# Kernel optimization log

Measured on AMD Instinct MI355X. Metric: run time of the kernel, lower is better.

## Reference

```python
import jax, jax.numpy as jnp
import numpy as np
import math

D, H, NQP, NKP = 512, 8, 4, 4
DH = D // H
OUT_DIM = D + H * NKP * 3  # 608


def setup_inputs() -> dict:
    key = jax.random.key(0)
    ks = jax.random.split(key, 12)
    B, L = 2, 1024
    s = jax.random.normal(ks[0], (B, L, D), dtype=jnp.float32)
    R = jax.random.normal(ks[1], (B, L, 3, 3), dtype=jnp.float32)
    tr = jax.random.normal(ks[2], (B, L, 3), dtype=jnp.float32)
    sc = 0.02
    Wq = jax.random.normal(ks[3], (D, D), dtype=jnp.float32) * sc
    Wk = jax.random.normal(ks[4], (D, D), dtype=jnp.float32) * sc
    Wv = jax.random.normal(ks[5], (D, D), dtype=jnp.float32) * sc
    Wqp = jax.random.normal(ks[6], (D, H * NQP * 3), dtype=jnp.float32) * sc
    Wkp = jax.random.normal(ks[7], (D, H * NKP * 3), dtype=jnp.float32) * sc
    Wvp = jax.random.normal(ks[8], (D, H * NKP * 3), dtype=jnp.float32) * sc
    Wo = jax.random.normal(ks[9], (OUT_DIM, D), dtype=jnp.float32) * sc
    bo = jnp.zeros((D,), dtype=jnp.float32)
    gamma = jnp.ones((D,), dtype=jnp.float32)
    beta = jnp.zeros((D,), dtype=jnp.float32)
    w_C = jnp.full((H,), math.log(20.0), dtype=jnp.float32)
    return dict(s=s, R=R, tr=tr, Wq=Wq, Wk=Wk, Wv=Wv, Wqp=Wqp, Wkp=Wkp,
                Wvp=Wvp, Wo=Wo, bo=bo, gamma=gamma, beta=beta, w_C=w_C)


def _layernorm(x, gamma, beta, eps=1e-5):
    mu = jnp.mean(x, axis=-1, keepdims=True)
    var = jnp.var(x, axis=-1, keepdims=True)
    return (x - mu) * jax.lax.rsqrt(var + eps) * gamma + beta


def reference(s, R, tr, Wq, Wk, Wv, Wqp, Wkp, Wvp, Wo, bo, gamma, beta, w_C):
    B, L, _ = s.shape
    # scalar q/k/v: (B, L, H, dh)
    Q = (s @ Wq).reshape(B, L, H, DH)
    K = (s @ Wk).reshape(B, L, H, DH)
    V = (s @ Wv).reshape(B, L, H, DH)
    a_s = jnp.einsum('bihd,bjhd->bhij', Q, K) / math.sqrt(DH)
    # local points: (B, L, H, P, 3)
    Qp = (s @ Wqp).reshape(B, L, H, NQP, 3)
    Kp = (s @ Wkp).reshape(B, L, H, NKP, 3)
    Vp = (s @ Wvp).reshape(B, L, H, NKP, 3)
    tr_e = tr[:, :, None, None, :]
    to_global = lambda p: jnp.einsum('blxy,blhpy->blhpx', R, p) + tr_e
    Qp_g, Kp_g, Vp_g = to_global(Qp), to_global(Kp), to_global(Vp)
    # (B, H, L, P, 3)
    qh = jnp.transpose(Qp_g, (0, 2, 1, 3, 4))
    kh = jnp.transpose(Kp_g, (0, 2, 1, 3, 4))
    diff = qh[:, :, :, None] - kh[:, :, None]          # (B,H,L,L,P,3)
    sq_dist = jnp.sum(diff * diff, axis=(-2, -1))      # (B,H,L,L)
    wc = jax.nn.softplus(w_C)[None, :, None, None]
    attn = jax.nn.softmax(a_s - 0.5 * wc * sq_dist, axis=-1)
    out_s = jnp.einsum('bhij,bjhd->bihd', attn, V).reshape(B, L, D)
    Vp_agg = jnp.einsum('bhij,bjhpc->bihpc', attn, Vp_g)  # (B,L,H,P,3)
    # global -> local: R^T (p - tr)
    Vp_local = jnp.einsum('blyx,blhpy->blhpx', R, Vp_agg - tr_e)
    out_p = Vp_local.reshape(B, L, H * NKP * 3)
    out = jnp.concatenate([out_s, out_p], axis=-1) @ Wo + bo
    return _layernorm(s + out, gamma, beta)
```

## Files before the change

### kernel.cpp

```cpp
#include <hip/hip_runtime.h>
#include <hip/hip_fp16.h>
#include <math.h>

typedef _Float16 f16;
typedef _Float16 f16x8 __attribute__((ext_vector_type(8)));
typedef _Float16 f16x4v __attribute__((ext_vector_type(4)));
typedef float f32x4 __attribute__((ext_vector_type(4)));

#define BATCH   2
#define LSEQ    1024
#define BLTOT   2048
#define DMODEL  512
#define NHEAD   8
#define PDIM    1824
#define AW      96
#define VW      80
#define ODIM    608
#define NSPLIT  2
#define OCPSTR  1310720

__global__ __launch_bounds__(256)
void prep_kernel(const float* __restrict__ s,
                 const float* __restrict__ Wq, const float* __restrict__ Wk,
                 const float* __restrict__ Wv, const float* __restrict__ Wqp,
                 const float* __restrict__ Wkp, const float* __restrict__ Wvp,
                 f16* __restrict__ sH, f16* __restrict__ WallT)
{
    const int blk = blockIdx.x;
    const int t = threadIdx.x;
    __shared__ float tile[32][33];

    if (blk < 1024) {
        const int i = blk * 256 + t;
        float4 v = ((const float4*)s)[i];
        f16x4v o = { (f16)v.x, (f16)v.y, (f16)v.z, (f16)v.w };
        ((f16x4v*)sH)[i] = o;
        return;
    }
    {
        const int idx = blk - 1024;
        const int n0 = (idx % 57) * 32, k0 = (idx / 57) * 32;
        const float* src; int ld, nc0;
        if      (n0 < 512)  { src = Wq;  ld = 512; nc0 = n0; }
        else if (n0 < 1024) { src = Wk;  ld = 512; nc0 = n0 - 512; }
        else if (n0 < 1536) { src = Wv;  ld = 512; nc0 = n0 - 1024; }
        else if (n0 < 1632) { src = Wqp; ld = 96;  nc0 = n0 - 1536; }
        else if (n0 < 1728) { src = Wkp; ld = 96;  nc0 = n0 - 1632; }
        else                { src = Wvp; ld = 96;  nc0 = n0 - 1728; }
#pragma unroll
        for (int i = 0; i < 4; ++i) {
            const int idx2 = t + i * 256;
            const int kl = idx2 >> 5, nl = idx2 & 31;
            tile[kl][nl] = src[(long long)(k0 + kl) * ld + nc0 + nl];
        }
        __syncthreads();
#pragma unroll
        for (int i = 0; i < 4; ++i) {
            const int idx2 = t + i * 256;
            const int nl = idx2 >> 5, kl = idx2 & 31;
            WallT[(long long)(n0 + nl) * 512 + k0 + kl] = (f16)tile[kl][nl];
        }
    }
}

__global__ __launch_bounds__(256)
void proj_kernel(const f16* __restrict__ A, const f16* __restrict__ Bt,
                 const float* __restrict__ Wo, f16* __restrict__ WoT,
                 f16* __restrict__ P)
{
    __shared__ f16 As[2][64][40];
    __shared__ f16 Bs[2][96][40];
    const int t = threadIdx.x;

    if (blockIdx.y >= 32) {
        float (*tile)[33] = (float(*)[33])&As[0][0][0];
        const int base = (blockIdx.x + (blockIdx.y - 32) * 19) * 8;
#pragma unroll 1
        for (int it = 0; it < 8; ++it) {
            const int idx = base + it;
            const int n0 = (idx & 15) * 32, k0 = (idx >> 4) * 32;
#pragma unroll
            for (int i = 0; i < 4; ++i) {
                const int idx2 = t + i * 256;
                const int kl = idx2 >> 5, nl = idx2 & 31;
                tile[kl][nl] = Wo[(long long)(k0 + kl) * 512 + n0 + nl];
            }
            __syncthreads();
#pragma unroll
            for (int i = 0; i < 4; ++i) {
                const int idx2 = t + i * 256;
                const int nl = idx2 >> 5, kl = idx2 & 31;
                WoT[(long long)(n0 + nl) * 608 + k0 + kl] = (f16)tile[kl][nl];
            }
            __syncthreads();
        }
        return;
    }

    const int w = t >> 6, lane = t & 63, l15 = lane & 15, lhi = lane >> 4;
    const int row0 = blockIdx.y * 64, col0 = blockIdx.x * 96;
    const int ar = t >> 2, ac = t & 3;
    const int K = 512;

    f32x4 acc[6];
#pragma unroll
    for (int n = 0; n < 6; ++n) acc[n] = (f32x4){0.f, 0.f, 0.f, 0.f};

    f16x8 aR, bR[2];
    aR = *(const f16x8*)&A[(long long)(row0 + ar) * K + ac * 8];
#pragma unroll
    for (int i = 0; i < 2; ++i) {
        const int cid = t + i * 256;
        if (cid < 384) {
            const int br = cid >> 2, bc = cid & 3;
            bR[i] = *(const f16x8*)&Bt[(long long)(col0 + br) * K + bc * 8];
        }
    }
    *(f16x8*)&As[0][ar][ac * 8] = aR;
#pragma unroll
    for (int i = 0; i < 2; ++i) {
        const int cid = t + i * 256;
        if (cid < 384) *(f16x8*)&Bs[0][cid >> 2][(cid & 3) * 8] = bR[i];
    }
    __syncthreads();

    for (int st = 0; st < 16; ++st) {
        const int cur = st & 1;
        if (st + 1 < 16) {
            const int k0 = (st + 1) << 5;
            aR = *(const f16x8*)&A[(long long)(row0 + ar) * K + k0 + ac * 8];
#pragma unroll
            for (int i = 0; i < 2; ++i) {
                const int cid = t + i * 256;
                if (cid < 384) {
                    const int br = cid >> 2, bc = cid & 3;
                    bR[i] = *(const f16x8*)&Bt[(long long)(col0 + br) * K + k0 + bc * 8];
                }
            }
        }
        f16x8 af = *(const f16x8*)&As[cur][w * 16 + l15][lhi * 8];
        f16x8 bf[6];
#pragma unroll
        for (int n = 0; n < 6; ++n)
            bf[n] = *(const f16x8*)&Bs[cur][n * 16 + l15][lhi * 8];
#pragma unroll
        for (int n = 0; n < 6; ++n)
            acc[n] = __builtin_amdgcn_mfma_f32_16x16x32_f16(af, bf[n], acc[n], 0, 0, 0);
        if (st + 1 < 16) {
            *(f16x8*)&As[cur ^ 1][ar][ac * 8] = aR;
#pragma unroll
            for (int i = 0; i < 2; ++i) {
                const int cid = t + i * 256;
                if (cid < 384) *(f16x8*)&Bs[cur ^ 1][cid >> 2][(cid & 3) * 8] = bR[i];
            }
        }
        __syncthreads();
    }

    const int row = row0 + w * 16 + lhi * 4;
#pragma unroll
    for (int n = 0; n < 6; ++n) {
        const int col = col0 + n * 16 + l15;
#pragma unroll
        for (int r = 0; r < 4; ++r)
            P[(long long)(row + r) * PDIM + col] = (f16)acc[n][r];
    }
}

template<int BN, bool OUT16>
__global__ __launch_bounds__(256)
void gemm2_kernel(const f16* __restrict__ A, const f16* __restrict__ Bt,
                  void* __restrict__ Cout, int K, int ldc)
{
    constexpr int BCH = (BN * 4 + 255) / 256;
    __shared__ f16 As[2][64][40];
    __shared__ f16 Bs[2][BN][40];
    const int t = threadIdx.x;
    const int w = t >> 6, lane = t & 63, l15 = lane & 15, lhi = lane >> 4;
    const int row0 = blockIdx.y * 64, col0 = blockIdx.x * BN;
    const int ar = t >> 2, ac = t & 3;

    f32x4 acc[BN / 16];
#pragma unroll
    for (int n = 0; n < BN / 16; ++n) acc[n] = (f32x4){0.f, 0.f, 0.f, 0.f};

    const int nsteps = K >> 5;

    f16x8 aR;
    f16x8 bR[BCH];
    aR = *(const f16x8*)&A[(long long)(row0 + ar) * K + ac * 8];
#pragma unroll
    for (int i = 0; i < BCH; ++i) {
        const int cid = t + i * 256;
        if (cid < BN * 4) {
            const int br = cid >> 2, bc = cid & 3;
            bR[i] = *(const f16x8*)&Bt[(long long)(col0 + br) * K + bc * 8];
        }
    }
    *(f16x8*)&As[0][ar][ac * 8] = aR;
#pragma unroll
    for (int i = 0; i < BCH; ++i) {
        const int cid = t + i * 256;
        if (cid < BN * 4) *(f16x8*)&Bs[0][cid >> 2][(cid & 3) * 8] = bR[i];
    }
    __syncthreads();

    for (int st = 0; st < nsteps; ++st) {
        const int cur = st & 1;
        if (st + 1 < nsteps) {
            const int k0 = (st + 1) << 5;
            aR = *(const f16x8*)&A[(long long)(row0 + ar) * K + k0 + ac * 8];
#pragma unroll
            for (int i = 0; i < BCH; ++i) {
                const int cid = t + i * 256;
                if (cid < BN * 4) {
                    const int br = cid >> 2, bc = cid & 3;
                    bR[i] = *(const f16x8*)&Bt[(long long)(col0 + br) * K + k0 + bc * 8];
                }
            }
        }
        f16x8 af = *(const f16x8*)&As[cur][w * 16 + l15][lhi * 8];
        f16x8 bf[BN / 16];
#pragma unroll
        for (int n = 0; n < BN / 16; ++n)
            bf[n] = *(const f16x8*)&Bs[cur][n * 16 + l15][lhi * 8];
#pragma unroll
        for (int n = 0; n < BN / 16; ++n)
            acc[n] = __builtin_amdgcn_mfma_f32_16x16x32_f16(af, bf[n], acc[n], 0, 0, 0);
        if (st + 1 < nsteps) {
            *(f16x8*)&As[cur ^ 1][ar][ac * 8] = aR;
#pragma unroll
            for (int i = 0; i < BCH; ++i) {
                const int cid = t + i * 256;
                if (cid < BN * 4) *(f16x8*)&Bs[cur ^ 1][cid >> 2][(cid & 3) * 8] = bR[i];
            }
        }
        __syncthreads();
    }

    const int row = row0 + w * 16 + lhi * 4;
#pragma unroll
    for (int n = 0; n < BN / 16; ++n) {
        const int col = col0 + n * 16 + l15;
#pragma unroll
        for (int r = 0; r < 4; ++r) {
            if (OUT16) ((f16*)Cout)[(long long)(row + r) * ldc + col] = (f16)acc[n][r];
            else       ((float*)Cout)[(long long)(row + r) * ldc + col] = acc[n][r];
        }
    }
}

__global__ __launch_bounds__(256)
void build_aug2_kernel(const f16* __restrict__ P, const float* __restrict__ Rm,
                       const float* __restrict__ tr, const float* __restrict__ wC,
                       f16* __restrict__ QA, f16* __restrict__ KA,
                       f16* __restrict__ VCT, float* __restrict__ KOFF)
{
    const int l0 = blockIdx.x * 64;
    const int bh = blockIdx.y;
    const int b = bh >> 3, h = bh & 7;
    const int t = threadIdx.x;

    __shared__ float Rl[64][9];
    __shared__ float trl[64][3];
    __shared__ f16 gq[64][12];
    __shared__ f16 gk[64][12];
    __shared__ float k2[64][4];
    __shared__ f16 Vt[VW][72];
    __shared__ float wcs;

    const long long blbase = (long long)b * LSEQ + l0;

    for (int i = t; i < 64 * 9; i += 256) Rl[i / 9][i % 9] = Rm[blbase * 9 + i];
    for (int i = t; i < 64 * 3; i += 256) trl[i / 3][i % 3] = tr[blbase * 3 + i];
    if (t == 0) { float x = wC[h]; wcs = log1pf(expf(x)); }
    __syncthreads();
    const float wc = wcs;

    for (int i = t; i < 768; i += 256) {
        const int l = i / 12, pp = i - l * 12;
        const int proj = pp >> 2, p = pp & 3;
        const f16* src = P + (blbase + l) * PDIM + 1536 + proj * 96 + h * 12 + p * 3;
        const float x = (float)src[0], y = (float)src[1], z = (float)src[2];
        const float gx = Rl[l][0]*x + Rl[l][1]*y + Rl[l][2]*z + trl[l][0];
        const float gy = Rl[l][3]*x + Rl[l][4]*y + Rl[l][5]*z + trl[l][1];
        const float gz = Rl[l][6]*x + Rl[l][7]*y + Rl[l][8]*z + trl[l][2];
        if (proj == 0) {
            gq[l][p * 3 + 0] = (f16)(wc * gx);
            gq[l][p * 3 + 1] = (f16)(wc * gy);
            gq[l][p * 3 + 2] = (f16)(wc * gz);
        } else if (proj == 1) {
            gk[l][p * 3 + 0] = (f16)gx;
            gk[l][p * 3 + 1] = (f16)gy;
            gk[l][p * 3 + 2] = (f16)gz;
            k2[l][p] = gx * gx + gy * gy + gz * gz;
        } else {
            Vt[64 + p * 3 + 0][l] = (f16)gx;
            Vt[64 + p * 3 + 1][l] = (f16)gy;
            Vt[64 + p * 3 + 2][l] = (f16)gz;
        }
    }
    for (int i = t; i < 512; i += 256) {
        const int l = i >> 3, ch = i & 7;
        f16x8 v = *(const f16x8*)&P[(blbase + l) * PDIM + 1024 + h * 64 + ch * 8];
#pragma unroll
        for (int j = 0; j < 8; ++j) Vt[ch * 8 + j][l] = v[j];
    }
    for (int i = t; i < 36; i += 256) {
        const int r = 76 + i / 9, ch = i % 9;
        *(f16x8*)&Vt[r][ch * 8] = (f16x8){0,0,0,0,0,0,0,0};
    }
    __syncthreads();

    if (t < 64)
        KOFF[(long long)bh * LSEQ + l0 + t] =
            0.5f * wc * (k2[t][0] + k2[t][1] + k2[t][2] + k2[t][3]);

    for (int i = t; i < 768; i += 256) {
        const int l = i / 12, ch = i - l * 12;
        const long long prow = (blbase + l) * PDIM;
        const long long orow = ((long long)bh * LSEQ + l0 + l) * AW;
        f16x8 q, k;
        if (ch < 8) {
            f16x8 qv = *(const f16x8*)&P[prow + h * 64 + ch * 8];
            f16x8 kv = *(const f16x8*)&P[prow + 512 + h * 64 + ch * 8];
            q = qv * (f16)0.125f;
            k = kv;
        } else if (ch == 8) {
#pragma unroll
            for (int j = 0; j < 8; ++j) { q[j] = gq[l][j]; k[j] = gk[l][j]; }
        } else if (ch == 9) {
#pragma unroll
            for (int j = 0; j < 8; ++j) {
                q[j] = (j < 4) ? gq[l][8 + j] : (f16)0.f;
                k[j] = (j < 4) ? gk[l][8 + j] : (f16)0.f;
            }
        } else {
            q = (f16x8){0,0,0,0,0,0,0,0};
            k = (f16x8){0,0,0,0,0,0,0,0};
        }
        *(f16x8*)&QA[orow + ch * 8] = q;
        *(f16x8*)&KA[orow + ch * 8] = k;
    }
    for (int i = t; i < 640; i += 256) {
        const int c = i >> 3, lg = i & 7;
        *(f16x8*)&VCT[((long long)bh * VW + c) * LSEQ + l0 + lg * 8] =
            *(const f16x8*)&Vt[c][lg * 8];
    }
}

__global__ __launch_bounds__(256, 2)
void attn_kernel(const f16* __restrict__ QA, const f16* __restrict__ KA,
                 const f16* __restrict__ VCT, const float* __restrict__ KOFF,
                 f16* __restrict__ OCp, float* __restrict__ LSE)
{
    const int bh = blockIdx.y;
    const int q0 = blockIdx.x * 64;
    const int z  = blockIdx.z;
    const int t = threadIdx.x;
    const int w = t >> 6, lane = t & 63, l15 = lane & 15, lhi = lane >> 4;

    __shared__ f16 Ks[128][104];
    __shared__ f16 Vs[VW][136];
    __shared__ f16 Ps[64][136];

    const f16* qbase = QA + ((long long)bh * LSEQ + q0 + w * 16 + l15) * AW;
    f16x8 qf[3];
#pragma unroll
    for (int ks = 0; ks < 3; ++ks)
        qf[ks] = *(const f16x8*)(qbase + ks * 32 + lhi * 8);

    f32x4 Oacc[5];
#pragma unroll
    for (int nv = 0; nv < 5; ++nv) Oacc[nv] = (f32x4){0.f, 0.f, 0.f, 0.f};
    float M = -1e30f, L = 0.f;

    const f16* kgbase = KA + (long long)bh * LSEQ * AW;
    const f16* vgbase = VCT + (long long)bh * VW * LSEQ;
    const float* koffb = KOFF + (long long)bh * LSEQ;

    const int kvbeg = z * (LSEQ / NSPLIT);
    const int kvend = kvbeg + LSEQ / NSPLIT;

#pragma unroll
    for (int i = 0; i < 6; ++i) {
        const int cid = t + i * 256;
        const int r = cid / 12, c = cid - r * 12;
        *(f16x8*)&Ks[r][c * 8] = *(const f16x8*)(kgbase + (long long)(kvbeg + r) * AW + c * 8);
    }
#pragma unroll
    for (int i = 0; i < 5; ++i) {
        const int cid = t + i * 256;
        const int r = cid >> 4, c = cid & 15;
        *(f16x8*)&Vs[r][c * 8] = *(const f16x8*)(vgbase + (long long)r * LSEQ + kvbeg + c * 8);
    }
    __syncthreads();

    for (int kv0 = kvbeg; kv0 < kvend; kv0 += 128) {
        const bool more = (kv0 + 128 < kvend);
        f16x8 kpre[6], vpre[5];
        if (more) {
#pragma unroll
            for (int i = 0; i < 6; ++i) {
                const int cid = t + i * 256;
                const int r = cid / 12, c = cid - r * 12;
                kpre[i] = *(const f16x8*)(kgbase + (long long)(kv0 + 128 + r) * AW + c * 8);
            }
#pragma unroll
            for (int i = 0; i < 5; ++i) {
                const int cid = t + i * 256;
                const int r = cid >> 4, c = cid & 15;
                vpre[i] = *(const f16x8*)(vgbase + (long long)r * LSEQ + kv0 + 128 + c * 8);
            }
        }

        f32x4 sc[8];
#pragma unroll
        for (int n = 0; n < 8; ++n) sc[n] = (f32x4){0.f, 0.f, 0.f, 0.f};
        __builtin_amdgcn_s_setprio(1);
#pragma unroll
        for (int n = 0; n < 8; ++n)
#pragma unroll
            for (int ks = 0; ks < 3; ++ks) {
                f16x8 kb = *(const f16x8*)&Ks[n * 16 + l15][ks * 32 + lhi * 8];
                sc[n] = __builtin_amdgcn_mfma_f32_16x16x32_f16(kb, qf[ks], sc[n], 0, 0, 0);
            }
        __builtin_amdgcn_s_setprio(0);
#pragma unroll
        for (int n = 0; n < 8; ++n) {
            const float4 ko4 = *(const float4*)&koffb[kv0 + n * 16 + lhi * 4];
            sc[n][0] -= ko4.x; sc[n][1] -= ko4.y; sc[n][2] -= ko4.z; sc[n][3] -= ko4.w;
        }
        float mr = sc[0][0];
#pragma unroll
        for (int n = 0; n < 8; ++n)
#pragma unroll
            for (int r = 0; r < 4; ++r) mr = fmaxf(mr, sc[n][r]);
        mr = fmaxf(mr, __shfl_xor(mr, 16));
        mr = fmaxf(mr, __shfl_xor(mr, 32));

        const bool nog = (mr <= M + 8.f);
        float rsum = 0.f;
        if (__all(nog)) {
#pragma unroll
            for (int n = 0; n < 8; ++n)
#pragma unroll
                for (int r = 0; r < 4; ++r) {
                    const float p = __expf(sc[n][r] - M);
                    sc[n][r] = p;
                    rsum += p;
                }
            rsum += __shfl_xor(rsum, 16);
            rsum += __shfl_xor(rsum, 32);
            L += rsum;
        } else {
            const float nm = fmaxf(M, mr);
            const float ss = __expf(M - nm);
            M = nm;
#pragma unroll
            for (int n = 0; n < 8; ++n)
#pragma unroll
                for (int r = 0; r < 4; ++r) {
                    const float p = __expf(sc[n][r] - M);
                    sc[n][r] = p;
                    rsum += p;
                }
            rsum += __shfl_xor(rsum, 16);
            rsum += __shfl_xor(rsum, 32);
            L = L * ss + rsum;
            float sr[4];
#pragma unroll
            for (int r = 0; r < 4; ++r) sr[r] = __shfl(ss, lhi * 4 + r);
#pragma unroll
            for (int nv = 0; nv < 5; ++nv)
#pragma unroll
                for (int r = 0; r < 4; ++r) Oacc[nv][r] *= sr[r];
        }

#pragma unroll
        for (int n = 0; n < 8; ++n) {
            f16x4v pv = { (f16)sc[n][0], (f16)sc[n][1], (f16)sc[n][2], (f16)sc[n][3] };
            *(f16x4v*)&Ps[w * 16 + l15][n * 16 + lhi * 4] = pv;
        }

        f16x8 pa[4];
#pragma unroll
        for (int ks = 0; ks < 4; ++ks)
            pa[ks] = *(const f16x8*)&Ps[w * 16 + l15][ks * 32 + lhi * 8];
        __builtin_amdgcn_s_setprio(1);
#pragma unroll
        for (int nv = 0; nv < 5; ++nv)
#pragma unroll
            for (int ks = 0; ks < 4; ++ks) {
                f16x8 vb = *(const f16x8*)&Vs[nv * 16 + l15][ks * 32 + lhi * 8];
                Oacc[nv] = __builtin_amdgcn_mfma_f32_16x16x32_f16(pa[ks], vb, Oacc[nv], 0, 0, 0);
            }
        __builtin_amdgcn_s_setprio(0);
        __syncthreads();

        if (more) {
#pragma unroll
            for (int i = 0; i < 6; ++i) {
                const int cid = t + i * 256;
                const int r = cid / 12, c = cid - r * 12;
                *(f16x8*)&Ks[r][c * 8] = kpre[i];
            }
#pragma unroll
            for (int i = 0; i < 5; ++i) {
                const int cid = t + i * 256;
                const int r = cid >> 4, c = cid & 15;
                *(f16x8*)&Vs[r][c * 8] = vpre[i];
            }
        }
        __syncthreads();
    }

    float invr[4];
#pragma unroll
    for (int r = 0; r < 4; ++r) {
        const float Lr = __shfl(L, lhi * 4 + r);
        invr[r] = 1.0f / Lr;
    }
    f16* obase = OCp + (((long long)(z * 16 + bh) * LSEQ) + q0 + w * 16 + lhi * 4) * VW;
#pragma unroll
    for (int nv = 0; nv < 5; ++nv)
#pragma unroll
        for (int r = 0; r < 4; ++r)
            obase[r * VW + nv * 16 + l15] = (f16)(Oacc[nv][r] * invr[r]);
    if (lhi == 0) {
        LSE[(long long)(z * 16 + bh) * LSEQ + q0 + w * 16 + l15] = M + __logf(L);
    }
}

__global__ __launch_bounds__(256)
void combine_concat_kernel(const f16* __restrict__ OCp, const float* __restrict__ LSE,
                           const float* __restrict__ Rm, const float* __restrict__ tr,
                           f16* __restrict__ CC)
{
    const int bl0 = blockIdx.x * 4;
    const int b = bl0 >> 10;
    const int t = threadIdx.x;

    __shared__ float w1s[4][8], w2s[4][8];
    if (t < 32) {
        const int row = t >> 3, h = t & 7;
        const int l = (bl0 + row) & 1023;
        const int bh = b * 8 + h;
        const float l1 = LSE[(long long)bh * LSEQ + l];
        const float l2 = LSE[(long long)(16 + bh) * LSEQ + l];
        const float mm = fmaxf(l1, l2);
        const float e1 = __expf(l1 - mm), e2 = __expf(l2 - mm);
        const float inv = 1.0f / (e1 + e2);
        w1s[row][h] = e1 * inv; w2s[row][h] = e2 * inv;
    }
    __syncthreads();

    for (int idx = t; idx < 2048; idx += 256) {
        const int row = idx >> 9, c = idx & 511;
        const int h = c >> 6, ch = c & 63;
        const int l = (bl0 + row) & 1023;
        const long long base = ((long long)(b * 8 + h) * LSEQ + l) * VW + ch;
        const float v = w1s[row][h] * (float)OCp[base] + w2s[row][h] * (float)OCp[OCPSTR + base];
        CC[(long long)(bl0 + row) * ODIM + c] = (f16)v;
    }
    if (t < 128) {
        const int row = t >> 5, h = (t >> 2) & 7, p = t & 3;
        const int bl = bl0 + row, l = bl & 1023;
        const long long base = ((long long)(b * 8 + h) * LSEQ + l) * VW + 64 + p * 3;
        const float w1 = w1s[row][h], w2 = w2s[row][h];
        float o[3];
#pragma unroll
        for (int c = 0; c < 3; ++c)
            o[c] = w1 * (float)OCp[base + c] + w2 * (float)OCp[OCPSTR + base + c]
                 - tr[(long long)bl * 3 + c];
        const float* Rr = Rm + (long long)bl * 9;
        f16* crow = CC + (long long)bl * ODIM + 512 + h * 12 + p * 3;
        crow[0] = (f16)(Rr[0]*o[0] + Rr[3]*o[1] + Rr[6]*o[2]);
        crow[1] = (f16)(Rr[1]*o[0] + Rr[4]*o[1] + Rr[7]*o[2]);
        crow[2] = (f16)(Rr[2]*o[0] + Rr[5]*o[1] + Rr[8]*o[2]);
    }
}

__global__ __launch_bounds__(256)
void residual_ln_kernel(const float* __restrict__ s, const float* __restrict__ Y,
                        const float* __restrict__ bo, const float* __restrict__ gamma,
                        const float* __restrict__ beta, float* __restrict__ out)
{
    const int bl = blockIdx.x;
    const int t = threadIdx.x;
    const float* srow = s + (long long)bl * DMODEL;
    const float* yrow = Y + (long long)bl * DMODEL;

    const float v0 = srow[t]       + yrow[t]       + bo[t];
    const float v1 = srow[t + 256] + yrow[t + 256] + bo[t + 256];

    float sum = v0 + v1, sq = v0 * v0 + v1 * v1;
#pragma unroll
    for (int o = 32; o > 0; o >>= 1) {
        sum += __shfl_xor(sum, o);
        sq  += __shfl_xor(sq,  o);
    }
    __shared__ float rs[4], rq[4];
    const int wid = t >> 6, lane = t & 63;
    if (lane == 0) { rs[wid] = sum; rq[wid] = sq; }
    __syncthreads();
    sum = rs[0] + rs[1] + rs[2] + rs[3];
    sq  = rq[0] + rq[1] + rq[2] + rq[3];

    const float mu  = sum * (1.0f / DMODEL);
    const float var = sq * (1.0f / DMODEL) - mu * mu;
    const float inv = rsqrtf(var + 1e-5f);

    out[(long long)bl * DMODEL + t]       = (v0 - mu) * inv * gamma[t]       + beta[t];
    out[(long long)bl * DMODEL + t + 256] = (v1 - mu) * inv * gamma[t + 256] + beta[t + 256];
}

extern "C" void kernel_launch(void* const* d_in, const int* in_sizes, int n_in,
                              void* d_out, int out_size, void* d_ws, size_t ws_size,
                              hipStream_t stream)
{
    const float* s    = (const float*)d_in[0];
    const float* R    = (const float*)d_in[1];
    const float* tr   = (const float*)d_in[2];
    const float* Wq   = (const float*)d_in[3];
    const float* Wk   = (const float*)d_in[4];
    const float* Wv   = (const float*)d_in[5];
    const float* Wqp  = (const float*)d_in[6];
    const float* Wkp  = (const float*)d_in[7];
    const float* Wvp  = (const float*)d_in[8];
    const float* Wo   = (const float*)d_in[9];
    const float* bo   = (const float*)d_in[10];
    const float* gam  = (const float*)d_in[11];
    const float* bet  = (const float*)d_in[12];
    const float* wC   = (const float*)d_in[13];
    float* out = (float*)d_out;

    f16* sH    = (f16*)d_ws;
    f16* WallT = sH + 1048576;
    f16* WoT   = WallT + 933888;
    f16* P     = WoT + 311296;
    f16* QA    = P + 3735552;
    f16* KA    = QA + 1572864;
    f16* VCT   = KA + 1572864;
    float* KOFF = (float*)(VCT + 1310720);
    f16* OCp    = (f16*)(KOFF + 16384);
    float* LSE  = (float*)(OCp + 2621440);
    f16* CC     = (f16*)(LSE + 32768);
    float* Y    = (float*)(CC + 1245184);

    const dim3 blk(256);

    prep_kernel<<<dim3(1936), blk, 0, stream>>>(s, Wq, Wk, Wv, Wqp, Wkp, Wvp,
                                                sH, WallT);

    proj_kernel<<<dim3(19, 34), blk, 0, stream>>>(sH, WallT, Wo, WoT, P);

    build_aug2_kernel<<<dim3(16, 16), blk, 0, stream>>>(P, R, tr, wC, QA, KA, VCT, KOFF);

    attn_kernel<<<dim3(16, 16, NSPLIT), blk, 0, stream>>>(QA, KA, VCT, KOFF, OCp, LSE);

    combine_concat_kernel<<<dim3(512), blk, 0, stream>>>(OCp, LSE, R, tr, CC);

    gemm2_kernel<64, false><<<dim3(8, 32), blk, 0, stream>>>(CC, WoT, Y, 608, 512);

    residual_ln_kernel<<<dim3(BLTOT), blk, 0, stream>>>(s, Y, bo, gam, bet, out);
}
```

Baseline: 70.81 us.

## Fuse split-KV combine into attention kernel via last-block atomic counter

Removes the separate combine_concat kernel. Each attention block now fences and bumps a per-tile atomic counter, and whichever of the two split blocks finishes second merges the two partial outputs using the LSE weights. That block also applies the inverse rotation to the point outputs and writes the concatenated CC buffer. This saves one kernel launch and a separate pass over OCp/LSE, at the cost of atomics, fences and a serial tail in the last-finishing block. The counters are reset in prep_kernel.

```diff
diff --git a/kernel.cpp b/kernel.cpp
--- a/kernel.cpp
+++ b/kernel.cpp
@@ -24,13 +24,15 @@
                  const float* __restrict__ Wq, const float* __restrict__ Wk,
                  const float* __restrict__ Wv, const float* __restrict__ Wqp,
                  const float* __restrict__ Wkp, const float* __restrict__ Wvp,
-                 f16* __restrict__ sH, f16* __restrict__ WallT)
+                 f16* __restrict__ sH, f16* __restrict__ WallT,
+                 int* __restrict__ cnt)
 {
     const int blk = blockIdx.x;
     const int t = threadIdx.x;
     __shared__ float tile[32][33];
 
     if (blk < 1024) {
+        if (blk == 0) cnt[t] = 0;
         const int i = blk * 256 + t;
         float4 v = ((const float4*)s)[i];
         f16x4v o = { (f16)v.x, (f16)v.y, (f16)v.z, (f16)v.w };
@@ -352,7 +354,9 @@
 __global__ __launch_bounds__(256, 2)
 void attn_kernel(const f16* __restrict__ QA, const f16* __restrict__ KA,
                  const f16* __restrict__ VCT, const float* __restrict__ KOFF,
-                 f16* __restrict__ OCp, float* __restrict__ LSE)
+                 const float* __restrict__ Rm, const float* __restrict__ trv,
+                 f16* __restrict__ OCp, float* __restrict__ LSE,
+                 int* __restrict__ cnt, f16* __restrict__ CC)
 {
     const int bh = blockIdx.y;
     const int q0 = blockIdx.x * 64;
@@ -530,51 +534,48 @@
     if (lhi == 0) {
         LSE[(long long)(z * 16 + bh) * LSEQ + q0 + w * 16 + l15] = M + __logf(L);
     }
-}
-
-__global__ __launch_bounds__(256)
-void combine_concat_kernel(const f16* __restrict__ OCp, const float* __restrict__ LSE,
-                           const float* __restrict__ Rm, const float* __restrict__ tr,
-                           f16* __restrict__ CC)
-{
-    const int bl0 = blockIdx.x * 4;
-    const int b = bl0 >> 10;
-    const int t = threadIdx.x;
-
-    __shared__ float w1s[4][8], w2s[4][8];
-    if (t < 32) {
-        const int row = t >> 3, h = t & 7;
-        const int l = (bl0 + row) & 1023;
-        const int bh = b * 8 + h;
-        const float l1 = LSE[(long long)bh * LSEQ + l];
-        const float l2 = LSE[(long long)(16 + bh) * LSEQ + l];
+
+    __shared__ int who;
+    __shared__ float w1s[64], w2s[64];
+    __threadfence();
+    __syncthreads();
+    if (t == 0) who = atomicAdd(&cnt[blockIdx.x * 16 + bh], 1);
+    __syncthreads();
+    if (who == 0) return;
+    __threadfence();
+
+    const int b = bh >> 3, h = bh & 7;
+    const long long blbase = (long long)b * LSEQ + q0;
+    if (t < 64) {
+        const float l1 = LSE[(long long)bh * LSEQ + q0 + t];
+        const float l2 = LSE[(long long)(16 + bh) * LSEQ + q0 + t];
         const float mm = fmaxf(l1, l2);
         const float e1 = __expf(l1 - mm), e2 = __expf(l2 - mm);
         const float inv = 1.0f / (e1 + e2);
-        w1s[row][h] = e1 * inv; w2s[row][h] = e2 * inv;
-    }
-    __syncthreads();
-
-    for (int idx = t; idx < 2048; idx += 256) {
-        const int row = idx >> 9, c = idx & 511;
-        const int h = c >> 6, ch = c & 63;
-        const int l = (bl0 + row) & 1023;
-        const long long base = ((long long)(b * 8 + h) * LSEQ + l) * VW + ch;
-        const float v = w1s[row][h] * (float)OCp[base] + w2s[row][h] * (float)OCp[OCPSTR + base];
-        CC[(long long)(bl0 + row) * ODIM + c] = (f16)v;
-    }
-    if (t < 128) {
-        const int row = t >> 5, h = (t >> 2) & 7, p = t & 3;
-        const int bl = bl0 + row, l = bl & 1023;
-        const long long base = ((long long)(b * 8 + h) * LSEQ + l) * VW + 64 + p * 3;
-        const float w1 = w1s[row][h], w2 = w2s[row][h];
+        w1s[t] = e1 * inv; w2s[t] = e2 * inv;
+    }
+    __syncthreads();
+    const f16* p1base = OCp + ((long long)bh * LSEQ + q0) * VW;
+    const f16* p2base = OCp + OCPSTR + ((long long)bh * LSEQ + q0) * VW;
+    for (int idx = t; idx < 64 * 64; idx += 256) {
+        const int row = idx >> 6, c = idx & 63;
+        const float v = w1s[row] * (float)p1base[row * VW + c]
+                      + w2s[row] * (float)p2base[row * VW + c];
+        CC[(blbase + row) * ODIM + h * 64 + c] = (f16)v;
+    }
+    {
+        const int i = t >> 2, p = t & 3;
+        const long long bl = blbase + i;
         float o[3];
 #pragma unroll
-        for (int c = 0; c < 3; ++c)
-            o[c] = w1 * (float)OCp[base + c] + w2 * (float)OCp[OCPSTR + base + c]
-                 - tr[(long long)bl * 3 + c];
-        const float* Rr = Rm + (long long)bl * 9;
-        f16* crow = CC + (long long)bl * ODIM + 512 + h * 12 + p * 3;
+        for (int c = 0; c < 3; ++c) {
+            const int ch = 64 + p * 3 + c;
+            o[c] = w1s[i] * (float)p1base[i * VW + ch]
+                 + w2s[i] * (float)p2base[i * VW + ch]
+                 - trv[bl * 3 + c];
+        }
+        const float* Rr = Rm + bl * 9;
+        f16* crow = CC + bl * ODIM + 512 + h * 12 + p * 3;
         crow[0] = (f16)(Rr[0]*o[0] + Rr[3]*o[1] + Rr[6]*o[2]);
         crow[1] = (f16)(Rr[1]*o[0] + Rr[4]*o[1] + Rr[7]*o[2]);
         crow[2] = (f16)(Rr[2]*o[0] + Rr[5]*o[1] + Rr[8]*o[2]);
@@ -647,19 +648,19 @@
     float* LSE  = (float*)(OCp + 2621440);
     f16* CC     = (f16*)(LSE + 32768);
     float* Y    = (float*)(CC + 1245184);
+    int* cnt    = (int*)(Y + 1048576);
 
     const dim3 blk(256);
 
     prep_kernel<<<dim3(1936), blk, 0, stream>>>(s, Wq, Wk, Wv, Wqp, Wkp, Wvp,
-                                                sH, WallT);
+                                                sH, WallT, cnt);
 
     proj_kernel<<<dim3(19, 34), blk, 0, stream>>>(sH, WallT, Wo, WoT, P);
 
     build_aug2_kernel<<<dim3(16, 16), blk, 0, stream>>>(P, R, tr, wC, QA, KA, VCT, KOFF);
 
-    attn_kernel<<<dim3(16, 16, NSPLIT), blk, 0, stream>>>(QA, KA, VCT, KOFF, OCp, LSE);
-
-    combine_concat_kernel<<<dim3(512), blk, 0, stream>>>(OCp, LSE, R, tr, CC);
+    attn_kernel<<<dim3(16, 16, NSPLIT), blk, 0, stream>>>(QA, KA, VCT, KOFF, R, tr,
+                                                          OCp, LSE, cnt, CC);
 
     gemm2_kernel<64, false><<<dim3(8, 32), blk, 0, stream>>>(CC, WoT, Y, 608, 512);
 
```

New measurement: 141.6 us. +100.0%, slower.

## Fuse s fp16 conversion into projection GEMM and fold key offset into QK

Applied to the files above, without the earlier changes.

The projection GEMM now reads the fp32 activations directly and converts them to fp16 while staging into shared memory. This removes the separate conversion pass and its sH buffer. The per-key distance offset is no longer kept as a separate array subtracted after the QK MFMA. Instead it is encoded as extra augmented dimensions: query ones times the negated key offset, split into a hi/lo fp16 pair, so the subtraction happens inside the matmul. The trade-offs are twice the global A-load bytes in the GEMM and some precision risk in representing the offset as two fp16 values.

```diff
diff --git a/kernel.cpp b/kernel.cpp
--- a/kernel.cpp
+++ b/kernel.cpp
@@ -20,51 +20,40 @@
 #define OCPSTR  1310720
 
 __global__ __launch_bounds__(256)
-void prep_kernel(const float* __restrict__ s,
-                 const float* __restrict__ Wq, const float* __restrict__ Wk,
+void prep_kernel(const float* __restrict__ Wq, const float* __restrict__ Wk,
                  const float* __restrict__ Wv, const float* __restrict__ Wqp,
                  const float* __restrict__ Wkp, const float* __restrict__ Wvp,
-                 f16* __restrict__ sH, f16* __restrict__ WallT)
+                 f16* __restrict__ WallT)
 {
     const int blk = blockIdx.x;
     const int t = threadIdx.x;
     __shared__ float tile[32][33];
 
-    if (blk < 1024) {
-        const int i = blk * 256 + t;
-        float4 v = ((const float4*)s)[i];
-        f16x4v o = { (f16)v.x, (f16)v.y, (f16)v.z, (f16)v.w };
-        ((f16x4v*)sH)[i] = o;
-        return;
-    }
-    {
-        const int idx = blk - 1024;
-        const int n0 = (idx % 57) * 32, k0 = (idx / 57) * 32;
-        const float* src; int ld, nc0;
-        if      (n0 < 512)  { src = Wq;  ld = 512; nc0 = n0; }
-        else if (n0 < 1024) { src = Wk;  ld = 512; nc0 = n0 - 512; }
-        else if (n0 < 1536) { src = Wv;  ld = 512; nc0 = n0 - 1024; }
-        else if (n0 < 1632) { src = Wqp; ld = 96;  nc0 = n0 - 1536; }
-        else if (n0 < 1728) { src = Wkp; ld = 96;  nc0 = n0 - 1632; }
-        else                { src = Wvp; ld = 96;  nc0 = n0 - 1728; }
-#pragma unroll
-        for (int i = 0; i < 4; ++i) {
-            const int idx2 = t + i * 256;
-            const int kl = idx2 >> 5, nl = idx2 & 31;
-            tile[kl][nl] = src[(long long)(k0 + kl) * ld + nc0 + nl];
-        }
-        __syncthreads();
-#pragma unroll
-        for (int i = 0; i < 4; ++i) {
-            const int idx2 = t + i * 256;
-            const int nl = idx2 >> 5, kl = idx2 & 31;
-            WallT[(long long)(n0 + nl) * 512 + k0 + kl] = (f16)tile[kl][nl];
-        }
+    const int n0 = (blk % 57) * 32, k0 = (blk / 57) * 32;
+    const float* src; int ld, nc0;
+    if      (n0 < 512)  { src = Wq;  ld = 512; nc0 = n0; }
+    else if (n0 < 1024) { src = Wk;  ld = 512; nc0 = n0 - 512; }
+    else if (n0 < 1536) { src = Wv;  ld = 512; nc0 = n0 - 1024; }
+    else if (n0 < 1632) { src = Wqp; ld = 96;  nc0 = n0 - 1536; }
+    else if (n0 < 1728) { src = Wkp; ld = 96;  nc0 = n0 - 1632; }
+    else                { src = Wvp; ld = 96;  nc0 = n0 - 1728; }
+#pragma unroll
+    for (int i = 0; i < 4; ++i) {
+        const int idx2 = t + i * 256;
+        const int kl = idx2 >> 5, nl = idx2 & 31;
+        tile[kl][nl] = src[(long long)(k0 + kl) * ld + nc0 + nl];
+    }
+    __syncthreads();
+#pragma unroll
+    for (int i = 0; i < 4; ++i) {
+        const int idx2 = t + i * 256;
+        const int nl = idx2 >> 5, kl = idx2 & 31;
+        WallT[(long long)(n0 + nl) * 512 + k0 + kl] = (f16)tile[kl][nl];
     }
 }
 
 __global__ __launch_bounds__(256)
-void proj_kernel(const f16* __restrict__ A, const f16* __restrict__ Bt,
+void proj_kernel(const float* __restrict__ S, const f16* __restrict__ Bt,
                  const float* __restrict__ Wo, f16* __restrict__ WoT,
                  f16* __restrict__ P)
 {
@@ -106,8 +95,10 @@
 #pragma unroll
     for (int n = 0; n < 6; ++n) acc[n] = (f32x4){0.f, 0.f, 0.f, 0.f};
 
-    f16x8 aR, bR[2];
-    aR = *(const f16x8*)&A[(long long)(row0 + ar) * K + ac * 8];
+    float4 a0, a1;
+    f16x8 bR[2];
+    a0 = *(const float4*)&S[(long long)(row0 + ar) * K + ac * 8];
+    a1 = *(const float4*)&S[(long long)(row0 + ar) * K + ac * 8 + 4];
 #pragma unroll
     for (int i = 0; i < 2; ++i) {
         const int cid = t + i * 256;
@@ -116,7 +107,11 @@
             bR[i] = *(const f16x8*)&Bt[(long long)(col0 + br) * K + bc * 8];
         }
     }
-    *(f16x8*)&As[0][ar][ac * 8] = aR;
+    {
+        f16x8 v = { (f16)a0.x, (f16)a0.y, (f16)a0.z, (f16)a0.w,
+                    (f16)a1.x, (f16)a1.y, (f16)a1.z, (f16)a1.w };
+        *(f16x8*)&As[0][ar][ac * 8] = v;
+    }
 #pragma unroll
     for (int i = 0; i < 2; ++i) {
         const int cid = t + i * 256;
@@ -128,7 +123,8 @@
         const int cur = st & 1;
         if (st + 1 < 16) {
             const int k0 = (st + 1) << 5;
-            aR = *(const f16x8*)&A[(long long)(row0 + ar) * K + k0 + ac * 8];
+            a0 = *(const float4*)&S[(long long)(row0 + ar) * K + k0 + ac * 8];
+            a1 = *(const float4*)&S[(long long)(row0 + ar) * K + k0 + ac * 8 + 4];
 #pragma unroll
             for (int i = 0; i < 2; ++i) {
                 const int cid = t + i * 256;
@@ -147,7 +143,9 @@
         for (int n = 0; n < 6; ++n)
             acc[n] = __builtin_amdgcn_mfma_f32_16x16x32_f16(af, bf[n], acc[n], 0, 0, 0);
         if (st + 1 < 16) {
-            *(f16x8*)&As[cur ^ 1][ar][ac * 8] = aR;
+            f16x8 v = { (f16)a0.x, (f16)a0.y, (f16)a0.z, (f16)a0.w,
+                        (f16)a1.x, (f16)a1.y, (f16)a1.z, (f16)a1.w };
+            *(f16x8*)&As[cur ^ 1][ar][ac * 8] = v;
 #pragma unroll
             for (int i = 0; i < 2; ++i) {
                 const int cid = t + i * 256;
@@ -254,7 +252,7 @@
 void build_aug2_kernel(const f16* __restrict__ P, const float* __restrict__ Rm,
                        const float* __restrict__ tr, const float* __restrict__ wC,
                        f16* __restrict__ QA, f16* __restrict__ KA,
-                       f16* __restrict__ VCT, float* __restrict__ KOFF)
+                       f16* __restrict__ VCT)
 {
     const int l0 = blockIdx.x * 64;
     const int bh = blockIdx.y;
@@ -312,10 +310,6 @@
     }
     __syncthreads();
 
-    if (t < 64)
-        KOFF[(long long)bh * LSEQ + l0 + t] =
-            0.5f * wc * (k2[t][0] + k2[t][1] + k2[t][2] + k2[t][3]);
-
     for (int i = t; i < 768; i += 256) {
         const int l = i / 12, ch = i - l * 12;
         const long long prow = (blbase + l) * PDIM;
@@ -330,11 +324,15 @@
 #pragma unroll
             for (int j = 0; j < 8; ++j) { q[j] = gq[l][j]; k[j] = gk[l][j]; }
         } else if (ch == 9) {
-#pragma unroll
-            for (int j = 0; j < 8; ++j) {
-                q[j] = (j < 4) ? gq[l][8 + j] : (f16)0.f;
-                k[j] = (j < 4) ? gk[l][8 + j] : (f16)0.f;
-            }
+            const float koff = 0.5f * wc * (k2[l][0] + k2[l][1] + k2[l][2] + k2[l][3]);
+            const f16 kh = (f16)koff;
+            const float kres = koff - (float)kh;
+#pragma unroll
+            for (int j = 0; j < 4; ++j) { q[j] = gq[l][8 + j]; k[j] = gk[l][8 + j]; }
+            q[4] = (f16)1.f; k[4] = -kh;
+            q[5] = (f16)1.f; k[5] = (f16)(-kres);
+            q[6] = (f16)0.f; k[6] = (f16)0.f;
+            q[7] = (f16)0.f; k[7] = (f16)0.f;
         } else {
             q = (f16x8){0,0,0,0,0,0,0,0};
             k = (f16x8){0,0,0,0,0,0,0,0};
@@ -351,7 +349,7 @@
 
 __global__ __launch_bounds__(256, 2)
 void attn_kernel(const f16* __restrict__ QA, const f16* __restrict__ KA,
-                 const f16* __restrict__ VCT, const float* __restrict__ KOFF,
+                 const f16* __restrict__ VCT,
                  f16* __restrict__ OCp, float* __restrict__ LSE)
 {
     const int bh = blockIdx.y;
@@ -377,7 +375,6 @@
 
     const f16* kgbase = KA + (long long)bh * LSEQ * AW;
     const f16* vgbase = VCT + (long long)bh * VW * LSEQ;
-    const float* koffb = KOFF + (long long)bh * LSEQ;
 
     const int kvbeg = z * (LSEQ / NSPLIT);
     const int kvend = kvbeg + LSEQ / NSPLIT;
@@ -426,11 +423,7 @@
                 sc[n] = __builtin_amdgcn_mfma_f32_16x16x32_f16(kb, qf[ks], sc[n], 0, 0, 0);
             }
         __builtin_amdgcn_s_setprio(0);
-#pragma unroll
-        for (int n = 0; n < 8; ++n) {
-            const float4 ko4 = *(const float4*)&koffb[kv0 + n * 16 + lhi * 4];
-            sc[n][0] -= ko4.x; sc[n][1] -= ko4.y; sc[n][2] -= ko4.z; sc[n][3] -= ko4.w;
-        }
+
         float mr = sc[0][0];
 #pragma unroll
         for (int n = 0; n < 8; ++n)
@@ -635,29 +628,26 @@
     const float* wC   = (const float*)d_in[13];
     float* out = (float*)d_out;
 
-    f16* sH    = (f16*)d_ws;
-    f16* WallT = sH + 1048576;
+    f16* WallT = (f16*)d_ws;
     f16* WoT   = WallT + 933888;
     f16* P     = WoT + 311296;
     f16* QA    = P + 3735552;
     f16* KA    = QA + 1572864;
     f16* VCT   = KA + 1572864;
-    float* KOFF = (float*)(VCT + 1310720);
-    f16* OCp    = (f16*)(KOFF + 16384);
-    float* LSE  = (float*)(OCp + 2621440);
-    f16* CC     = (f16*)(LSE + 32768);
-    float* Y    = (float*)(CC + 1245184);
+    f16* OCp   = VCT + 1310720;
+    float* LSE = (float*)(OCp + 2621440);
+    f16* CC    = (f16*)(LSE + 32768);
+    float* Y   = (float*)(CC + 1245184);
 
     const dim3 blk(256);
 
-    prep_kernel<<<dim3(1936), blk, 0, stream>>>(s, Wq, Wk, Wv, Wqp, Wkp, Wvp,
-                                                sH, WallT);
-
-    proj_kernel<<<dim3(19, 34), blk, 0, stream>>>(sH, WallT, Wo, WoT, P);
-
-    build_aug2_kernel<<<dim3(16, 16), blk, 0, stream>>>(P, R, tr, wC, QA, KA, VCT, KOFF);
-
-    attn_kernel<<<dim3(16, 16, NSPLIT), blk, 0, stream>>>(QA, KA, VCT, KOFF, OCp, LSE);
+    prep_kernel<<<dim3(912), blk, 0, stream>>>(Wq, Wk, Wv, Wqp, Wkp, Wvp, WallT);
+
+    proj_kernel<<<dim3(19, 34), blk, 0, stream>>>(s, WallT, Wo, WoT, P);
+
+    build_aug2_kernel<<<dim3(16, 16), blk, 0, stream>>>(P, R, tr, wC, QA, KA, VCT);
+
+    attn_kernel<<<dim3(16, 16, NSPLIT), blk, 0, stream>>>(QA, KA, VCT, OCp, LSE);
 
     combine_concat_kernel<<<dim3(512), blk, 0, stream>>>(OCp, LSE, R, tr, CC);
 
```

Result: no change. 70.73 us, median of 2 (-0.1%).
